# Kernel tuning notes

Hardware: AMD Instinct MI355X
Metric: run time of the kernel (lower is better)

Reference implementation:

```python
import jax, jax.numpy as jnp
import numpy as np

N = 100000
E = 1600000
K = 2  # KProp steps


def setup_inputs() -> dict:
    key = jax.random.key(0)
    ks = jax.random.split(key, 8)
    x = jax.random.normal(ks[0], (N, 64), dtype=jnp.float32)
    edge_index = jax.random.randint(ks[1], (2, E), 0, N, dtype=jnp.int32)
    s = 1.0 / np.sqrt(64)
    W2l = jax.random.normal(ks[2], (64, 64), dtype=jnp.float32) * s
    W2r = jax.random.normal(ks[3], (64, 64), dtype=jnp.float32) * s
    b2 = jnp.zeros((64,), dtype=jnp.float32)
    W3l = jax.random.normal(ks[4], (64, 16), dtype=jnp.float32) * s
    W3r = jax.random.normal(ks[5], (64, 16), dtype=jnp.float32) * s
    b3 = jnp.zeros((16,), dtype=jnp.float32)
    return {"x": x, "edge_index": edge_index, "W2l": W2l, "W2r": W2r,
            "b2": b2, "W3l": W3l, "W3r": W3r, "b3": b3}


def reference(x, edge_index, W2l, W2r, b2, W3l, W3r, b3):
    dst, src = edge_index[0], edge_index[1]  # adj_t[i,j]: edge j -> i
    ones = jnp.ones((E,), dtype=x.dtype)
    deg = jax.ops.segment_sum(ones, dst, num_segments=N)  # in-degree
    dinv = jnp.where(deg > 0, jax.lax.rsqrt(jnp.maximum(deg, 1.0)), 0.0)
    w = dinv[dst] * dinv[src]  # gcn_norm weights (no self-loops in norm)

    # KProp: K steps of (D^-1/2 A D^-1/2 + I) @ h  (set_diag adds unit diag)
    h = x
    for _ in range(K):
        h = jax.ops.segment_sum(w[:, None] * h[src], dst, num_segments=N) + h

    degm = jnp.maximum(deg, 1.0)[:, None]

    # SAGEConv 1: mean-neighbor aggregate + root weight
    agg = jax.ops.segment_sum(h[src], dst, num_segments=N) / degm
    h = agg @ W2l + h @ W2r + b2
    h = jax.nn.selu(h)

    # SAGEConv 2
    agg = jax.ops.segment_sum(h[src], dst, num_segments=N) / degm
    h = agg @ W3l + h @ W3r + b3
    return jax.nn.softmax(h, axis=1)
```

## Files before the change

### kernel.cpp

```cpp
#include <hip/hip_runtime.h>
#include <hip/hip_bf16.h>

#define NNODES 100000
#define NEDGES 1600000
#define NBUCK 391
#define BCAP 4800
#define SPLIT_TILE 2048
#define NSPLIT ((NEDGES + SPLIT_TILE - 1) / SPLIT_TILE)

typedef short short8 __attribute__((ext_vector_type(8)));
typedef float floatx4 __attribute__((ext_vector_type(4)));

__device__ __forceinline__ void f4add(float4& a, const float4& v) {
    a.x += v.x; a.y += v.y; a.z += v.z; a.w += v.w;
}

__device__ __forceinline__ float4 b4tof4(ushort4 u) {
    return make_float4(__uint_as_float((unsigned)u.x << 16),
                       __uint_as_float((unsigned)u.y << 16),
                       __uint_as_float((unsigned)u.z << 16),
                       __uint_as_float((unsigned)u.w << 16));
}

__device__ __forceinline__ unsigned short f2b(float f) {
    unsigned u = __float_as_uint(f);
    u += 0x7fffu + ((u >> 16) & 1u);
    return (unsigned short)(u >> 16);
}

__global__ __launch_bounds__(256) void split_kernel(
    const int* __restrict__ dst, const int* __restrict__ src,
    int* __restrict__ gcur, unsigned* __restrict__ pairtmp) {
    __shared__ int lhist[NBUCK];
    __shared__ int lstart[NBUCK];
    __shared__ int ldst[SPLIT_TILE];
    int t = threadIdx.x;
    for (int i = t; i < NBUCK; i += 256) lhist[i] = 0;
    __syncthreads();
    int base = blockIdx.x * SPLIT_TILE;
    int n = min(SPLIT_TILE, NEDGES - base);
    for (int i = t; i < n; i += 256) {
        int d = dst[base + i];
        ldst[i] = d;
        atomicAdd(&lhist[d >> 8], 1);
    }
    __syncthreads();
    for (int i = t; i < NBUCK; i += 256) {
        int c = lhist[i];
        lstart[i] = (c > 0) ? atomicAdd(&gcur[i], c) : 0;
        lhist[i] = 0;
    }
    __syncthreads();
    for (int i = t; i < n; i += 256) {
        int d = ldst[i];
        int k = d >> 8;
        int s = src[base + i];
        int pos = lstart[k] + atomicAdd(&lhist[k], 1);
        pairtmp[(size_t)k * BCAP + pos] = ((unsigned)s << 8) | (unsigned)(d & 255);
    }
}

__global__ void bucketscan_kernel(const int* __restrict__ gcur, int* __restrict__ basearr) {
    __shared__ int lds[512];
    int t = threadIdx.x;
    int v = (t < NBUCK) ? gcur[t] : 0;
    lds[t] = v;
    __syncthreads();
    for (int s = 1; s < 512; s <<= 1) {
        int u = (t >= s) ? lds[t - s] : 0;
        __syncthreads();
        lds[t] += u;
        __syncthreads();
    }
    if (t < NBUCK) basearr[t] = lds[t] - v;
}

__global__ __launch_bounds__(256) void finalize_kernel(
    const unsigned* __restrict__ pairtmp, const int* __restrict__ gcur,
    const int* __restrict__ basearr, const float* __restrict__ x,
    int* __restrict__ col, int* __restrict__ deg, int* __restrict__ rowoff,
    float* __restrict__ dinv, unsigned short* __restrict__ g0b) {
    __shared__ int ldeg[256];
    __shared__ int lcur[256];
    __shared__ float ldi[256];
    __shared__ int lsc[256];
    int k = blockIdx.x;
    int t = threadIdx.x;
    int node0 = k << 8;
    int ncount = min(256, NNODES - node0);
    int base = basearr[k];
    int count = gcur[k];
    ldeg[t] = 0;
    __syncthreads();
    const unsigned* pb = pairtmp + (size_t)k * BCAP;
    for (int i = t; i < count; i += 256) {
        atomicAdd(&ldeg[pb[i] & 255], 1);
    }
    __syncthreads();
    int a = ldeg[t];
    lsc[t] = a;
    __syncthreads();
    for (int s = 1; s < 256; s <<= 1) {
        int v = (t >= s) ? lsc[t - s] : 0;
        __syncthreads();
        lsc[t] += v;
        __syncthreads();
    }
    int excl = lsc[t] - a;
    lcur[t] = base + excl;
    if (t < ncount) {
        int n0 = node0 + t;
        rowoff[n0] = base + excl;
        deg[n0] = a;
        float di = (a > 0) ? rsqrtf((float)a) : 0.0f;
        ldi[t] = di;
        dinv[n0] = di;
    }
    __syncthreads();
    for (int i = t; i < count; i += 256) {
        unsigned p = pb[i];
        int dl = (int)(p & 255u);
        int s = (int)(p >> 8);
        int pos = atomicAdd(&lcur[dl], 1);
        col[pos] = s;
    }
    const float4* x4 = (const float4*)x;
    int f4count = ncount * 16;
    int b4 = node0 * 16;
    for (int j = t; j < f4count; j += 256) {
        float di = ldi[j >> 4];
        float4 v = x4[b4 + j];
        ushort4 u;
        u.x = f2b(di * v.x); u.y = f2b(di * v.y);
        u.z = f2b(di * v.z); u.w = f2b(di * v.w);
        *(ushort4*)(g0b + (size_t)(b4 + j) * 4) = u;
    }
}

template <int MODE>
__global__ __launch_bounds__(256) void gatherw_kernel(
    const unsigned short* __restrict__ vin, const float* __restrict__ hin,
    float* __restrict__ outf, unsigned short* __restrict__ outb,
    const int* __restrict__ rowoff, const int* __restrict__ deg,
    const int* __restrict__ col, const float* __restrict__ dinv) {
    int node = blockIdx.x * 4 + (threadIdx.x >> 6);
    int lane = threadIdx.x & 63;
    int sub = lane & 15;
    int g = lane >> 4;
    int beg = rowoff[node];
    int dg = deg[node];
    int end = beg + dg;
    float4 a0 = {0.f, 0.f, 0.f, 0.f};
    float4 a1 = {0.f, 0.f, 0.f, 0.f};
    int e = beg + g;
    for (; e + 4 < end; e += 8) {
        int c0 = col[e];
        int c1 = col[e + 4];
        ushort4 u0 = *(const ushort4*)(vin + (size_t)c0 * 64 + sub * 4);
        ushort4 u1 = *(const ushort4*)(vin + (size_t)c1 * 64 + sub * 4);
        f4add(a0, b4tof4(u0));
        f4add(a1, b4tof4(u1));
    }
    if (e < end) {
        int c0 = col[e];
        ushort4 u0 = *(const ushort4*)(vin + (size_t)c0 * 64 + sub * 4);
        f4add(a0, b4tof4(u0));
    }
    f4add(a0, a1);
    a0.x += __shfl_xor(a0.x, 16); a0.y += __shfl_xor(a0.y, 16);
    a0.z += __shfl_xor(a0.z, 16); a0.w += __shfl_xor(a0.w, 16);
    a0.x += __shfl_xor(a0.x, 32); a0.y += __shfl_xor(a0.y, 32);
    a0.z += __shfl_xor(a0.z, 32); a0.w += __shfl_xor(a0.w, 32);
    if (lane < 16) {
        size_t off = (size_t)node * 64 + sub * 4;
        if (MODE <= 1) {
            float di = dinv[node];
            float4 h = *(const float4*)(hin + off);
            float4 hn = make_float4(h.x + di * a0.x, h.y + di * a0.y,
                                    h.z + di * a0.z, h.w + di * a0.w);
            if (MODE == 0) {
                *(float4*)(outf + off) = hn;
                ushort4 u;
                u.x = f2b(di * hn.x); u.y = f2b(di * hn.y);
                u.z = f2b(di * hn.z); u.w = f2b(di * hn.w);
                *(ushort4*)(outb + off) = u;
            } else {
                ushort4 u;
                u.x = f2b(hn.x); u.y = f2b(hn.y);
                u.z = f2b(hn.z); u.w = f2b(hn.w);
                *(ushort4*)(outb + off) = u;
            }
        } else {
            float r = 1.0f / (float)(dg > 0 ? dg : 1);
            ushort4 u;
            u.x = f2b(a0.x * r); u.y = f2b(a0.y * r);
            u.z = f2b(a0.z * r); u.w = f2b(a0.w * r);
            *(ushort4*)(outb + off) = u;
        }
    }
}

__global__ __launch_bounds__(256) void dense1_mfma(
    const unsigned short* __restrict__ aggb, const unsigned short* __restrict__ hb,
    unsigned short* __restrict__ h3b,
    const float* __restrict__ W2l, const float* __restrict__ W2r,
    const float* __restrict__ b2) {
    __shared__ unsigned short Wt[64 * 144];
    int t = threadIdx.x;
    for (int idx = t; idx < 128 * 64; idx += 256) {
        int k = idx >> 6, j = idx & 63;
        float v = (k < 64) ? W2l[k * 64 + j] : W2r[(k - 64) * 64 + j];
        Wt[j * 144 + k] = f2b(v);
    }
    __syncthreads();
    int wib = t >> 6, lane = t & 63;
    int tile = blockIdx.x * 4 + wib;
    if (tile * 16 >= NNODES) return;
    int node0 = tile * 16;
    int jj = lane & 15, kg = lane >> 4;
    short8 bfrag[4][4];
#pragma unroll
    for (int nt = 0; nt < 4; ++nt)
#pragma unroll
        for (int s = 0; s < 4; ++s)
            bfrag[nt][s] = *(const short8*)&Wt[(nt * 16 + jj) * 144 + s * 32 + kg * 8];
    int arow = node0 + jj;
    const unsigned short* ap = aggb + (size_t)arow * 64 + kg * 8;
    const unsigned short* hp = hb + (size_t)arow * 64 + kg * 8;
    short8 afrag[4];
    afrag[0] = *(const short8*)ap;
    afrag[1] = *(const short8*)(ap + 32);
    afrag[2] = *(const short8*)hp;
    afrag[3] = *(const short8*)(hp + 32);
    const float lam = 1.0507009873554804934193349852946f;
    const float alp = 1.6732632423543772848170429916717f;
#pragma unroll
    for (int nt = 0; nt < 4; ++nt) {
        floatx4 acc = {0.f, 0.f, 0.f, 0.f};
#pragma unroll
        for (int s = 0; s < 4; ++s)
            acc = __builtin_amdgcn_mfma_f32_16x16x32_bf16(afrag[s], bfrag[nt][s], acc, 0, 0, 0);
        float bias = b2[nt * 16 + jj];
#pragma unroll
        for (int r = 0; r < 4; ++r) {
            float v = acc[r] + bias;
            float o = (v > 0.0f) ? lam * v : lam * alp * expm1f(v);
            int node = node0 + kg * 4 + r;
            h3b[(size_t)node * 64 + nt * 16 + jj] = f2b(o);
        }
    }
}

__global__ __launch_bounds__(256) void dense2_mfma(
    const unsigned short* __restrict__ aggb, const unsigned short* __restrict__ hb,
    float* __restrict__ out,
    const float* __restrict__ W3l, const float* __restrict__ W3r,
    const float* __restrict__ b3) {
    __shared__ unsigned short Wt[16 * 144];
    int t = threadIdx.x;
    for (int idx = t; idx < 128 * 16; idx += 256) {
        int k = idx >> 4, j = idx & 15;
        float v = (k < 64) ? W3l[k * 16 + j] : W3r[(k - 64) * 16 + j];
        Wt[j * 144 + k] = f2b(v);
    }
    __syncthreads();
    int wib = t >> 6, lane = t & 63;
    int tile = blockIdx.x * 4 + wib;
    if (tile * 16 >= NNODES) return;
    int node0 = tile * 16;
    int jj = lane & 15, kg = lane >> 4;
    short8 bfrag[4];
#pragma unroll
    for (int s = 0; s < 4; ++s)
        bfrag[s] = *(const short8*)&Wt[jj * 144 + s * 32 + kg * 8];
    int arow = node0 + jj;
    const unsigned short* ap = aggb + (size_t)arow * 64 + kg * 8;
    const unsigned short* hp = hb + (size_t)arow * 64 + kg * 8;
    short8 afrag[4];
    afrag[0] = *(const short8*)ap;
    afrag[1] = *(const short8*)(ap + 32);
    afrag[2] = *(const short8*)hp;
    afrag[3] = *(const short8*)(hp + 32);
    floatx4 acc = {0.f, 0.f, 0.f, 0.f};
#pragma unroll
    for (int s = 0; s < 4; ++s)
        acc = __builtin_amdgcn_mfma_f32_16x16x32_bf16(afrag[s], bfrag[s], acc, 0, 0, 0);
    float bias = b3[jj];
#pragma unroll
    for (int r = 0; r < 4; ++r) {
        float v = acc[r] + bias;
        float m = v;
        m = fmaxf(m, __shfl_xor(m, 1));
        m = fmaxf(m, __shfl_xor(m, 2));
        m = fmaxf(m, __shfl_xor(m, 4));
        m = fmaxf(m, __shfl_xor(m, 8));
        float ex = expf(v - m);
        float s2 = ex;
        s2 += __shfl_xor(s2, 1);
        s2 += __shfl_xor(s2, 2);
        s2 += __shfl_xor(s2, 4);
        s2 += __shfl_xor(s2, 8);
        int node = node0 + kg * 4 + r;
        out[(size_t)node * 16 + jj] = ex / s2;
    }
}

extern "C" void kernel_launch(void* const* d_in, const int* in_sizes, int n_in,
                              void* d_out, int out_size, void* d_ws, size_t ws_size,
                              hipStream_t stream) {
    const float* x   = (const float*)d_in[0];
    const int*   ei  = (const int*)d_in[1];
    const float* W2l = (const float*)d_in[2];
    const float* W2r = (const float*)d_in[3];
    const float* b2  = (const float*)d_in[4];
    const float* W3l = (const float*)d_in[5];
    const float* W3r = (const float*)d_in[6];
    const float* b3  = (const float*)d_in[7];
    float* out = (float*)d_out;

    const int* dst = ei;
    const int* src = ei + NEDGES;

    char* ws = (char*)d_ws;
    float*          bufA = (float*)ws;          ws += (size_t)NNODES * 64 * 4;
    unsigned short* E0   = (unsigned short*)ws; ws += (size_t)NNODES * 64 * 2;
    unsigned short* E1   = (unsigned short*)ws; ws += (size_t)NNODES * 64 * 2;
    int*      col     = (int*)ws;      ws += (size_t)NEDGES * 4;
    int*      deg     = (int*)ws;      ws += (size_t)NNODES * 4;
    int*      rowoff  = (int*)ws;      ws += (size_t)NNODES * 4;
    float*    dinv    = (float*)ws;    ws += (size_t)NNODES * 4;
    int*      gcur    = (int*)ws;      ws += NBUCK * 4;
    int*      basearr = (int*)ws;      ws += NBUCK * 4;

    unsigned* pairtmp = (unsigned*)bufA;
    unsigned short* h3b = (unsigned short*)bufA;

    hipMemsetAsync(gcur, 0, NBUCK * 4, stream);

    split_kernel<<<NSPLIT, 256, 0, stream>>>(dst, src, gcur, pairtmp);
    bucketscan_kernel<<<1, 512, 0, stream>>>(gcur, basearr);
    finalize_kernel<<<NBUCK, 256, 0, stream>>>(pairtmp, gcur, basearr, x,
                                               col, deg, rowoff, dinv, E0);

    int nblk = NNODES / 4;
    int ndense = (NNODES / 16 + 3) / 4;
    gatherw_kernel<0><<<nblk, 256, 0, stream>>>(E0, x, bufA, E1, rowoff, deg, col, dinv);
    gatherw_kernel<1><<<nblk, 256, 0, stream>>>(E1, bufA, nullptr, E0, rowoff, deg, col, dinv);
    gatherw_kernel<2><<<nblk, 256, 0, stream>>>(E0, nullptr, nullptr, E1, rowoff, deg, col, dinv);
    dense1_mfma<<<ndense, 256, 0, stream>>>(E1, E0, h3b, W2l, W2r, b2);
    gatherw_kernel<2><<<nblk, 256, 0, stream>>>(h3b, nullptr, nullptr, E0, rowoff, deg, col, dinv);
    dense2_mfma<<<ndense, 256, 0, stream>>>(E0, h3b, out, W3l, W3r, b3);
}
```

Before: 352.9 us.

## Two-pass radix bucket split, 16-byte gathers, and bf16 intermediate h

Replaces the single 391-way bucket scatter with a two-level split: first into 25 coarse buckets, then each coarse bucket into 16 fine buckets. The aim is better write locality and fewer global atomics. The gather kernel now has 8 lanes per neighbour, each loading 16 bytes, instead of 16 lanes loading 8 bytes. The intermediate h after the first propagation step is stored as bf16 rather than fp32, which cuts its traffic and workspace but adds rounding error and one extra launch plus an extra pass over the edge pairs.

```diff
diff --git a/kernel.cpp b/kernel.cpp
--- a/kernel.cpp
+++ b/kernel.cpp
@@ -3,24 +3,17 @@
 
 #define NNODES 100000
 #define NEDGES 1600000
+#define NC 25
+#define CAP1 68000
 #define NBUCK 391
 #define BCAP 4800
 #define SPLIT_TILE 2048
 #define NSPLIT ((NEDGES + SPLIT_TILE - 1) / SPLIT_TILE)
+#define T2TILES 17
 
 typedef short short8 __attribute__((ext_vector_type(8)));
+typedef unsigned short ushx8 __attribute__((ext_vector_type(8)));
 typedef float floatx4 __attribute__((ext_vector_type(4)));
-
-__device__ __forceinline__ void f4add(float4& a, const float4& v) {
-    a.x += v.x; a.y += v.y; a.z += v.z; a.w += v.w;
-}
-
-__device__ __forceinline__ float4 b4tof4(ushort4 u) {
-    return make_float4(__uint_as_float((unsigned)u.x << 16),
-                       __uint_as_float((unsigned)u.y << 16),
-                       __uint_as_float((unsigned)u.z << 16),
-                       __uint_as_float((unsigned)u.w << 16));
-}
 
 __device__ __forceinline__ unsigned short f2b(float f) {
     unsigned u = __float_as_uint(f);
@@ -28,42 +21,84 @@
     return (unsigned short)(u >> 16);
 }
 
-__global__ __launch_bounds__(256) void split_kernel(
+__device__ __forceinline__ void acc8(float* a, ushx8 u) {
+#pragma unroll
+    for (int i = 0; i < 8; ++i)
+        a[i] += __uint_as_float((unsigned)u[i] << 16);
+}
+
+__global__ __launch_bounds__(256) void split1_kernel(
     const int* __restrict__ dst, const int* __restrict__ src,
-    int* __restrict__ gcur, unsigned* __restrict__ pairtmp) {
-    __shared__ int lhist[NBUCK];
-    __shared__ int lstart[NBUCK];
+    int* __restrict__ gcur1, unsigned* __restrict__ cpairs) {
+    __shared__ int lhist[NC];
+    __shared__ int lstart[NC];
     __shared__ int ldst[SPLIT_TILE];
     int t = threadIdx.x;
-    for (int i = t; i < NBUCK; i += 256) lhist[i] = 0;
+    if (t < NC) lhist[t] = 0;
     __syncthreads();
     int base = blockIdx.x * SPLIT_TILE;
     int n = min(SPLIT_TILE, NEDGES - base);
     for (int i = t; i < n; i += 256) {
         int d = dst[base + i];
         ldst[i] = d;
-        atomicAdd(&lhist[d >> 8], 1);
-    }
-    __syncthreads();
-    for (int i = t; i < NBUCK; i += 256) {
-        int c = lhist[i];
-        lstart[i] = (c > 0) ? atomicAdd(&gcur[i], c) : 0;
-        lhist[i] = 0;
+        atomicAdd(&lhist[d >> 12], 1);
+    }
+    __syncthreads();
+    if (t < NC) {
+        int c = lhist[t];
+        lstart[t] = (c > 0) ? atomicAdd(&gcur1[t], c) : 0;
+        lhist[t] = 0;
     }
     __syncthreads();
     for (int i = t; i < n; i += 256) {
         int d = ldst[i];
-        int k = d >> 8;
+        int k = d >> 12;
         int s = src[base + i];
         int pos = lstart[k] + atomicAdd(&lhist[k], 1);
-        pairtmp[(size_t)k * BCAP + pos] = ((unsigned)s << 8) | (unsigned)(d & 255);
-    }
-}
-
-__global__ void bucketscan_kernel(const int* __restrict__ gcur, int* __restrict__ basearr) {
+        cpairs[(size_t)k * CAP1 + pos] = ((unsigned)s << 12) | (unsigned)(d & 4095);
+    }
+}
+
+__global__ __launch_bounds__(256) void split2_kernel(
+    const unsigned* __restrict__ cpairs, const int* __restrict__ gcur1,
+    int* __restrict__ gcur2, unsigned* __restrict__ fpairs) {
+    int c = blockIdx.x / T2TILES;
+    int tile = blockIdx.x % T2TILES;
+    int cnt = gcur1[c];
+    int base = tile * 4096;
+    if (base >= cnt) return;
+    int n = min(4096, cnt - base);
+    __shared__ unsigned stash[4096];
+    __shared__ int lhist[16];
+    __shared__ int lstart[16];
+    int t = threadIdx.x;
+    if (t < 16) lhist[t] = 0;
+    __syncthreads();
+    const unsigned* pb = cpairs + (size_t)c * CAP1 + base;
+    for (int i = t; i < n; i += 256) {
+        unsigned p = pb[i];
+        stash[i] = p;
+        atomicAdd(&lhist[(p >> 8) & 15], 1);
+    }
+    __syncthreads();
+    if (t < 16) {
+        int cc = lhist[t];
+        lstart[t] = (cc > 0) ? atomicAdd(&gcur2[c * 16 + t], cc) : 0;
+        lhist[t] = 0;
+    }
+    __syncthreads();
+    for (int i = t; i < n; i += 256) {
+        unsigned p = stash[i];
+        int f = (p >> 8) & 15;
+        int pos = lstart[f] + atomicAdd(&lhist[f], 1);
+        fpairs[(size_t)(c * 16 + f) * BCAP + pos] = ((p >> 12) << 8) | (p & 255u);
+    }
+}
+
+__global__ void bucketscan_kernel(const int* __restrict__ gcur2, int* __restrict__ basearr) {
     __shared__ int lds[512];
     int t = threadIdx.x;
-    int v = (t < NBUCK) ? gcur[t] : 0;
+    int v = (t < NBUCK) ? gcur2[t] : 0;
     lds[t] = v;
     __syncthreads();
     for (int s = 1; s < 512; s <<= 1) {
@@ -76,7 +111,7 @@
 }
 
 __global__ __launch_bounds__(256) void finalize_kernel(
-    const unsigned* __restrict__ pairtmp, const int* __restrict__ gcur,
+    const unsigned* __restrict__ fpairs, const int* __restrict__ gcur2,
     const int* __restrict__ basearr, const float* __restrict__ x,
     int* __restrict__ col, int* __restrict__ deg, int* __restrict__ rowoff,
     float* __restrict__ dinv, unsigned short* __restrict__ g0b) {
@@ -89,10 +124,10 @@
     int node0 = k << 8;
     int ncount = min(256, NNODES - node0);
     int base = basearr[k];
-    int count = gcur[k];
+    int count = gcur2[k];
     ldeg[t] = 0;
     __syncthreads();
-    const unsigned* pb = pairtmp + (size_t)k * BCAP;
+    const unsigned* pb = fpairs + (size_t)k * BCAP;
     for (int i = t; i < count; i += 256) {
         atomicAdd(&ldeg[pb[i] & 255], 1);
     }
@@ -139,63 +174,72 @@
 
 template <int MODE>
 __global__ __launch_bounds__(256) void gatherw_kernel(
-    const unsigned short* __restrict__ vin, const float* __restrict__ hin,
-    float* __restrict__ outf, unsigned short* __restrict__ outb,
+    const unsigned short* __restrict__ vin, const float* __restrict__ hinf,
+    const unsigned short* __restrict__ hinb,
+    unsigned short* __restrict__ out0, unsigned short* __restrict__ out1,
     const int* __restrict__ rowoff, const int* __restrict__ deg,
     const int* __restrict__ col, const float* __restrict__ dinv) {
     int node = blockIdx.x * 4 + (threadIdx.x >> 6);
     int lane = threadIdx.x & 63;
-    int sub = lane & 15;
-    int g = lane >> 4;
+    int sub = lane & 7;
+    int g = lane >> 3;
     int beg = rowoff[node];
     int dg = deg[node];
     int end = beg + dg;
-    float4 a0 = {0.f, 0.f, 0.f, 0.f};
-    float4 a1 = {0.f, 0.f, 0.f, 0.f};
+    float af[8] = {0.f, 0.f, 0.f, 0.f, 0.f, 0.f, 0.f, 0.f};
+    float bf[8] = {0.f, 0.f, 0.f, 0.f, 0.f, 0.f, 0.f, 0.f};
     int e = beg + g;
-    for (; e + 4 < end; e += 8) {
+    for (; e + 8 < end; e += 16) {
         int c0 = col[e];
-        int c1 = col[e + 4];
-        ushort4 u0 = *(const ushort4*)(vin + (size_t)c0 * 64 + sub * 4);
-        ushort4 u1 = *(const ushort4*)(vin + (size_t)c1 * 64 + sub * 4);
-        f4add(a0, b4tof4(u0));
-        f4add(a1, b4tof4(u1));
+        int c1 = col[e + 8];
+        ushx8 u0 = *(const ushx8*)(vin + (size_t)c0 * 64 + sub * 8);
+        ushx8 u1 = *(const ushx8*)(vin + (size_t)c1 * 64 + sub * 8);
+        acc8(af, u0);
+        acc8(bf, u1);
     }
     if (e < end) {
         int c0 = col[e];
-        ushort4 u0 = *(const ushort4*)(vin + (size_t)c0 * 64 + sub * 4);
-        f4add(a0, b4tof4(u0));
-    }
-    f4add(a0, a1);
-    a0.x += __shfl_xor(a0.x, 16); a0.y += __shfl_xor(a0.y, 16);
-    a0.z += __shfl_xor(a0.z, 16); a0.w += __shfl_xor(a0.w, 16);
-    a0.x += __shfl_xor(a0.x, 32); a0.y += __shfl_xor(a0.y, 32);
-    a0.z += __shfl_xor(a0.z, 32); a0.w += __shfl_xor(a0.w, 32);
-    if (lane < 16) {
-        size_t off = (size_t)node * 64 + sub * 4;
+        ushx8 u0 = *(const ushx8*)(vin + (size_t)c0 * 64 + sub * 8);
+        acc8(af, u0);
+    }
+#pragma unroll
+    for (int i = 0; i < 8; ++i) {
+        float v = af[i] + bf[i];
+        v += __shfl_xor(v, 8);
+        v += __shfl_xor(v, 16);
+        v += __shfl_xor(v, 32);
+        af[i] = v;
+    }
+    if (lane < 8) {
+        size_t off = (size_t)node * 64 + lane * 8;
         if (MODE <= 1) {
             float di = dinv[node];
-            float4 h = *(const float4*)(hin + off);
-            float4 hn = make_float4(h.x + di * a0.x, h.y + di * a0.y,
-                                    h.z + di * a0.z, h.w + di * a0.w);
+            float hv[8];
             if (MODE == 0) {
-                *(float4*)(outf + off) = hn;
-                ushort4 u;
-                u.x = f2b(di * hn.x); u.y = f2b(di * hn.y);
-                u.z = f2b(di * hn.z); u.w = f2b(di * hn.w);
-                *(ushort4*)(outb + off) = u;
+                float4 h0 = *(const float4*)(hinf + off);
+                float4 h1 = *(const float4*)(hinf + off + 4);
+                hv[0] = h0.x; hv[1] = h0.y; hv[2] = h0.z; hv[3] = h0.w;
+                hv[4] = h1.x; hv[5] = h1.y; hv[6] = h1.z; hv[7] = h1.w;
             } else {
-                ushort4 u;
-                u.x = f2b(hn.x); u.y = f2b(hn.y);
-                u.z = f2b(hn.z); u.w = f2b(hn.w);
-                *(ushort4*)(outb + off) = u;
+                ushx8 u = *(const ushx8*)(hinb + off);
+#pragma unroll
+                for (int i = 0; i < 8; ++i) hv[i] = __uint_as_float((unsigned)u[i] << 16);
             }
+            ushx8 uh, ug;
+#pragma unroll
+            for (int i = 0; i < 8; ++i) {
+                float hn = hv[i] + di * af[i];
+                uh[i] = f2b(hn);
+                if (MODE == 0) ug[i] = f2b(di * hn);
+            }
+            *(ushx8*)(out0 + off) = uh;
+            if (MODE == 0) *(ushx8*)(out1 + off) = ug;
         } else {
             float r = 1.0f / (float)(dg > 0 ? dg : 1);
-            ushort4 u;
-            u.x = f2b(a0.x * r); u.y = f2b(a0.y * r);
-            u.z = f2b(a0.z * r); u.w = f2b(a0.w * r);
-            *(ushort4*)(outb + off) = u;
+            ushx8 u;
+#pragma unroll
+            for (int i = 0; i < 8; ++i) u[i] = f2b(af[i] * r);
+            *(ushx8*)(out0 + off) = u;
         }
     }
 }
@@ -322,32 +366,34 @@
     const int* src = ei + NEDGES;
 
     char* ws = (char*)d_ws;
-    float*          bufA = (float*)ws;          ws += (size_t)NNODES * 64 * 4;
-    unsigned short* E0   = (unsigned short*)ws; ws += (size_t)NNODES * 64 * 2;
-    unsigned short* E1   = (unsigned short*)ws; ws += (size_t)NNODES * 64 * 2;
+    unsigned short* B0 = (unsigned short*)ws; ws += (size_t)NNODES * 64 * 2;
+    unsigned short* B1 = (unsigned short*)ws; ws += (size_t)NNODES * 64 * 2;
+    unsigned short* B2 = (unsigned short*)ws; ws += (size_t)NNODES * 64 * 2;
     int*      col     = (int*)ws;      ws += (size_t)NEDGES * 4;
     int*      deg     = (int*)ws;      ws += (size_t)NNODES * 4;
     int*      rowoff  = (int*)ws;      ws += (size_t)NNODES * 4;
     float*    dinv    = (float*)ws;    ws += (size_t)NNODES * 4;
-    int*      gcur    = (int*)ws;      ws += NBUCK * 4;
+    int*      gcur1   = (int*)ws;      ws += NC * 4;
+    int*      gcur2   = (int*)ws;      ws += NBUCK * 4;
     int*      basearr = (int*)ws;      ws += NBUCK * 4;
 
-    unsigned* pairtmp = (unsigned*)bufA;
-    unsigned short* h3b = (unsigned short*)bufA;
-
-    hipMemsetAsync(gcur, 0, NBUCK * 4, stream);
-
-    split_kernel<<<NSPLIT, 256, 0, stream>>>(dst, src, gcur, pairtmp);
-    bucketscan_kernel<<<1, 512, 0, stream>>>(gcur, basearr);
-    finalize_kernel<<<NBUCK, 256, 0, stream>>>(pairtmp, gcur, basearr, x,
-                                               col, deg, rowoff, dinv, E0);
+    unsigned* cpairs = (unsigned*)B1;
+    unsigned* fpairs = (unsigned*)B2;
+
+    hipMemsetAsync(gcur1, 0, (NC + NBUCK) * 4, stream);
+
+    split1_kernel<<<NSPLIT, 256, 0, stream>>>(dst, src, gcur1, cpairs);
+    split2_kernel<<<NC * T2TILES, 256, 0, stream>>>(cpairs, gcur1, gcur2, fpairs);
+    bucketscan_kernel<<<1, 512, 0, stream>>>(gcur2, basearr);
+    finalize_kernel<<<NBUCK, 256, 0, stream>>>(fpairs, gcur2, basearr, x,
+                                               col, deg, rowoff, dinv, B0);
 
     int nblk = NNODES / 4;
     int ndense = (NNODES / 16 + 3) / 4;
-    gatherw_kernel<0><<<nblk, 256, 0, stream>>>(E0, x, bufA, E1, rowoff, deg, col, dinv);
-    gatherw_kernel<1><<<nblk, 256, 0, stream>>>(E1, bufA, nullptr, E0, rowoff, deg, col, dinv);
-    gatherw_kernel<2><<<nblk, 256, 0, stream>>>(E0, nullptr, nullptr, E1, rowoff, deg, col, dinv);
-    dense1_mfma<<<ndense, 256, 0, stream>>>(E1, E0, h3b, W2l, W2r, b2);
-    gatherw_kernel<2><<<nblk, 256, 0, stream>>>(h3b, nullptr, nullptr, E0, rowoff, deg, col, dinv);
-    dense2_mfma<<<ndense, 256, 0, stream>>>(E0, h3b, out, W3l, W3r, b3);
-}
+    gatherw_kernel<0><<<nblk, 256, 0, stream>>>(B0, x, nullptr, B1, B2, rowoff, deg, col, dinv);
+    gatherw_kernel<1><<<nblk, 256, 0, stream>>>(B2, nullptr, B1, B0, nullptr, rowoff, deg, col, dinv);
+    gatherw_kernel<2><<<nblk, 256, 0, stream>>>(B0, nullptr, nullptr, B1, nullptr, rowoff, deg, col, dinv);
+    dense1_mfma<<<ndense, 256, 0, stream>>>(B1, B0, B2, W2l, W2r, b2);
+    gatherw_kernel<2><<<nblk, 256, 0, stream>>>(B2, nullptr, nullptr, B0, nullptr, rowoff, deg, col, dinv);
+    dense2_mfma<<<ndense, 256, 0, stream>>>(B0, B2, out, W3l, W3r, b3);
+}
```

Result: faster. 327.7 us (-7.1%).
